# Kernel tuning notes

Hardware: AMD Instinct MI355X
Metric: run time of the kernel (lower is better)

Reference implementation:

```python
import jax, jax.numpy as jnp
import numpy as np

GRID_NUM = 3  # pykan 'grid' (number of intervals)
K = 3         # spline order

def bspline_basis(x, grid, k):
    # Cox-de Boor recursion, matching pykan B_batch with a shared extended grid.
    # x: (N, Din); grid: (G,) extended grid with G = GRID_NUM + 2*k + 1
    x = x[..., None]  # (N, Din, 1)
    B = ((x >= grid[:-1]) & (x < grid[1:])).astype(x.dtype)  # (N, Din, G-1)
    for p in range(1, k + 1):
        left = (x - grid[:-(p + 1)]) / (grid[p:-1] - grid[:-(p + 1)])
        right = (grid[p + 1:] - x) / (grid[p + 1:] - grid[1:-p])
        B = left * B[..., :-1] + right * B[..., 1:]
    return B  # (N, Din, GRID_NUM + k)

def setup_inputs() -> dict:
    key = jax.random.key(0)
    k1, k2, k3 = jax.random.split(key, 3)
    Bsz, S, Din, Dout = 4, 2048, 768, 768
    x = jax.random.normal(k1, (Bsz, S, Din), dtype=jnp.float32)
    # noise-scale-like init for spline coefficients (noise_scale=0.1)
    coef = (0.1 / GRID_NUM) * jax.random.normal(k2, (Dout, Din, GRID_NUM + K), dtype=jnp.float32)
    inv_sqrt_in = np.float32(1.0 / np.sqrt(Din))
    scale_base = inv_sqrt_in + 0.1 * inv_sqrt_in * jax.random.normal(k3, (Dout, Din), dtype=jnp.float32)
    scale_sp = jnp.ones((Dout, Din), dtype=jnp.float32)
    bias = jnp.zeros((Dout,), dtype=jnp.float32)
    return {"x": x, "coef": coef, "scale_base": scale_base, "scale_sp": scale_sp, "bias": bias}

def reference(x, coef, scale_base, scale_sp, bias):
    # x: (B, S, Din) -> flatten tokens as the original module does
    Bsz, S, Din = x.shape
    xf = x.reshape(-1, Din)  # (N, Din)
    # extended grid: linspace(-1,1,GRID_NUM+1) extended by K points each side (h = 2/GRID_NUM)
    h = 2.0 / GRID_NUM
    grid = jnp.arange(-K, GRID_NUM + K + 1, dtype=x.dtype) * h - 1.0  # (GRID_NUM + 2K + 1,)
    basis = bspline_basis(xf, grid, K)  # (N, Din, GRID_NUM+K)
    # per-edge activation: scale_base*silu(x) + scale_sp*spline(x); mask==1; symbolic branch==0
    base = jax.nn.silu(xf) @ scale_base.T  # (N, Dout)
    spline = jnp.einsum('nim,oim->no', basis, scale_sp[:, :, None] * coef)  # (N, Dout)
    out = base + spline + bias  # bias from pykan biases[l].weight
    return out.reshape(Bsz, S, -1)
```

## Files before the change

kernel.cpp:

```cpp
#include <hip/hip_runtime.h>


typedef _Float16 f16;
typedef __attribute__((ext_vector_type(4))) _Float16 f16x4;
typedef __attribute__((ext_vector_type(8))) _Float16 f16x8;
typedef __attribute__((ext_vector_type(4))) float f32x4;

#define NTOK 8192
#define DIN 768
#define DOUT 768
#define KAUG 5376
#define BM 64
#define BN 128
#define BK 32
#define KT (KAUG / BK)
#define NBLK ((NTOK / BM) * (DOUT / BN))

typedef __attribute__((address_space(1))) void gvoid;
typedef __attribute__((address_space(3))) void lvoid;

__device__ __forceinline__ void spline6(float xv, float* __restrict__ B, float& s) {
  s = xv / (1.0f + __expf(-xv));
  const float h = 2.0f / 3.0f;
  float Bb[9];
#pragma unroll
  for (int g = 0; g < 9; ++g) {
    float t0 = (float)(g - 3) * h - 1.0f;
    float t1 = (float)(g - 2) * h - 1.0f;
    Bb[g] = (xv >= t0 && xv < t1) ? 1.0f : 0.0f;
  }
#pragma unroll
  for (int p = 1; p <= 3; ++p) {
    float inv = 1.0f / ((float)p * h);
#pragma unroll
    for (int j = 0; j < 8; ++j) {
      if (j < 9 - p) {
        float tj = (float)(j - 3) * h - 1.0f;
        float tjp1 = (float)(j + p + 1 - 3) * h - 1.0f;
        Bb[j] = (xv - tj) * inv * Bb[j] + (tjp1 - xv) * inv * Bb[j + 1];
      }
    }
  }
#pragma unroll
  for (int m = 0; m < 6; ++m) B[m] = Bb[m];
}

__global__ __launch_bounds__(256) void build_A(const float* __restrict__ x,
                                               f16* __restrict__ Aa) {
  int idx = (blockIdx.x * 256 + threadIdx.x) * 4;
  float4 xv = *(const float4*)(x + idx);
  int n = idx / DIN;
  int i = idx - n * DIN;

  float B0[6], B1[6], B2[6], B3[6];
  float s0, s1, s2, s3;
  spline6(xv.x, B0, s0);
  spline6(xv.y, B1, s1);
  spline6(xv.z, B2, s2);
  spline6(xv.w, B3, s3);

  size_t base = (size_t)n * KAUG + i;
  f16x4 sv = {(f16)s0, (f16)s1, (f16)s2, (f16)s3};
  *(f16x4*)(Aa + base) = sv;
#pragma unroll
  for (int m = 0; m < 6; ++m) {
    f16x4 bv = {(f16)B0[m], (f16)B1[m], (f16)B2[m], (f16)B3[m]};
    *(f16x4*)(Aa + base + (size_t)(m + 1) * DIN) = bv;
  }
}

__global__ __launch_bounds__(256) void build_W(const float* __restrict__ sb,
                                               const float* __restrict__ ssp,
                                               const float* __restrict__ coef,
                                               f16* __restrict__ Wa) {
  int idx = blockIdx.x * 256 + threadIdx.x;
  float b = sb[idx];
  float sp = ssp[idx];
  int o = idx / DIN;
  int i = idx - o * DIN;
  size_t base = (size_t)o * KAUG + i;
  Wa[base] = (f16)b;
#pragma unroll
  for (int m = 0; m < 6; ++m)
    Wa[base + (size_t)(m + 1) * DIN] = (f16)(sp * coef[(size_t)idx * 6 + m]);
}

__global__ __launch_bounds__(256) void kan_gemm(const f16* __restrict__ A,
                                                const f16* __restrict__ W,
                                                const float* __restrict__ bias,
                                                float* __restrict__ out) {
  __shared__ alignas(16) f16 As0[BM * BK];
  __shared__ alignas(16) f16 As1[BM * BK];
  __shared__ alignas(16) f16 Bs0[BN * BK];
  __shared__ alignas(16) f16 Bs1[BN * BK];

  const int tid = threadIdx.x;
  const int wave = tid >> 6;
  const int lane = tid & 63;

  const int bid = blockIdx.x;
  const int wg = (bid & 7) * (NBLK / 8) + (bid >> 3);
  const int col = wg % 6;
  const int panel = wg / 6;
  const int m0 = panel * BM;
  const int n0 = col * BN;

  const int wm = (wave >> 1) * 32;
  const int wn = (wave & 1) * 64;
  const int r = lane & 15;
  const int q = lane >> 4;

  f32x4 acc[2][4] = {};

  const int c0 = wave * 64 + lane;
  const int rowS0 = c0 >> 2, kb0 = c0 & 3;
  const int c1 = c0 + 256;
  const int rowS1 = c1 >> 2, kb1 = c1 & 3;

  const f16* gA0 = A + (size_t)(m0 + rowS0) * KAUG + kb0 * 8;
  const f16* gB0 = W + (size_t)(n0 + rowS0) * KAUG + kb0 * 8;
  const f16* gB1 = W + (size_t)(n0 + rowS1) * KAUG + kb1 * 8;

  const int wo = wave * 512;

#define STAGE(AS, BS, ktile)                                                             \
  do {                                                                                   \
    const int koff = (ktile)*BK;                                                         \
    __builtin_amdgcn_global_load_lds((gvoid*)(gA0 + koff), (lvoid*)(AS + wo), 16, 0, 0); \
    __builtin_amdgcn_global_load_lds((gvoid*)(gB0 + koff), (lvoid*)(BS + wo), 16, 0, 0); \
    __builtin_amdgcn_global_load_lds((gvoid*)(gB1 + koff), (lvoid*)(BS + wo + 2048), 16, \
                                     0, 0);                                              \
  } while (0)

#define COMPUTE(AS, BS)                                                                  \
  do {                                                                                   \
    f16x8 af[2], bf[4];                                                                  \
    _Pragma("unroll") for (int mi = 0; mi < 2; ++mi) af[mi] =                            \
        *(const f16x8*)&AS[(wm + mi * 16 + r) * BK + q * 8];                             \
    _Pragma("unroll") for (int ni = 0; ni < 4; ++ni) bf[ni] =                            \
        *(const f16x8*)&BS[(wn + ni * 16 + r) * BK + q * 8];                             \
    _Pragma("unroll") for (int mi = 0; mi < 2; ++mi) _Pragma("unroll") for (int ni = 0;  \
                                                                            ni < 4;     \
                                                                            ++ni)       \
        acc[mi][ni] =                                                                    \
        __builtin_amdgcn_mfma_f32_16x16x32_f16(af[mi], bf[ni], acc[mi][ni], 0, 0, 0);    \
  } while (0)

  STAGE(As0, Bs0, 0);
  __syncthreads();

  for (int kt = 0; kt < KT; kt += 2) {
    STAGE(As1, Bs1, kt + 1);
    COMPUTE(As0, Bs0);
    __syncthreads();
    if (kt + 2 < KT) STAGE(As0, Bs0, kt + 2);
    COMPUTE(As1, Bs1);
    __syncthreads();
  }

#undef STAGE
#undef COMPUTE

#pragma unroll
  for (int mi = 0; mi < 2; ++mi) {
#pragma unroll
    for (int ni = 0; ni < 4; ++ni) {
      const int gcol = n0 + wn + ni * 16 + r;
      const float bv = bias[gcol];
#pragma unroll
      for (int rg = 0; rg < 4; ++rg) {
        const int grow = m0 + wm + mi * 16 + q * 4 + rg;
        out[(size_t)grow * DOUT + gcol] = acc[mi][ni][rg] + bv;
      }
    }
  }
}

extern "C" void kernel_launch(void* const* d_in, const int* in_sizes, int n_in,
                              void* d_out, int out_size, void* d_ws, size_t ws_size,
                              hipStream_t stream) {
  const float* x = (const float*)d_in[0];
  const float* coef = (const float*)d_in[1];
  const float* scale_base = (const float*)d_in[2];
  const float* scale_sp = (const float*)d_in[3];
  const float* bias = (const float*)d_in[4];
  float* out = (float*)d_out;

  f16* Aa = (f16*)d_ws;
  f16* Wa = (f16*)((char*)d_ws + (size_t)NTOK * KAUG * 2);

  build_A<<<(NTOK * DIN) / (256 * 4), 256, 0, stream>>>(x, Aa);
  build_W<<<(DOUT * DIN) / 256, 256, 0, stream>>>(scale_base, scale_sp, coef, Wa);
  kan_gemm<<<NBLK, 256, 0, stream>>>(Aa, Wa, bias, out);
}
```

Before: 212.1 us.

## Enlarge GEMM tiles, add triple-buffered pipeline with LDS swizzle, merge prep kernels

The GEMM moves to 128x192x64 tiles with 512 threads and a three-stage LDS ring buffer. Global-to-LDS loads are issued two tiles ahead and split across the half-K phases, with XOR-swizzled LDS layout to avoid bank conflicts and setprio around MFMA bursts. The two preprocessing kernels are merged into one launch, and the W build now uses vectorized loads. This aims to raise arithmetic intensity and hide memory latency, at the cost of more LDS and register pressure and fewer blocks (256) on the machine.

```diff
diff --git a/kernel.cpp b/kernel.cpp
--- a/kernel.cpp
+++ b/kernel.cpp
@@ -2,6 +2,7 @@
 
 
 typedef _Float16 f16;
+typedef __attribute__((ext_vector_type(2))) _Float16 f16x2;
 typedef __attribute__((ext_vector_type(4))) _Float16 f16x4;
 typedef __attribute__((ext_vector_type(8))) _Float16 f16x8;
 typedef __attribute__((ext_vector_type(4))) float f32x4;
@@ -10,10 +11,12 @@
 #define DIN 768
 #define DOUT 768
 #define KAUG 5376
-#define BM 64
-#define BN 128
-#define BK 32
-#define KT (KAUG / BK)
+#define BM 128
+#define BN 192
+#define BK 64
+#define NKT (KAUG / BK)
+#define ASZ (BM * BK)
+#define BSZ (BN * BK)
 #define NBLK ((NTOK / BM) * (DOUT / BN))
 
 typedef __attribute__((address_space(1))) void gvoid;
@@ -45,54 +48,65 @@
   for (int m = 0; m < 6; ++m) B[m] = Bb[m];
 }
 
-__global__ __launch_bounds__(256) void build_A(const float* __restrict__ x,
-                                               f16* __restrict__ Aa) {
-  int idx = (blockIdx.x * 256 + threadIdx.x) * 4;
-  float4 xv = *(const float4*)(x + idx);
-  int n = idx / DIN;
-  int i = idx - n * DIN;
-
-  float B0[6], B1[6], B2[6], B3[6];
-  float s0, s1, s2, s3;
-  spline6(xv.x, B0, s0);
-  spline6(xv.y, B1, s1);
-  spline6(xv.z, B2, s2);
-  spline6(xv.w, B3, s3);
-
-  size_t base = (size_t)n * KAUG + i;
-  f16x4 sv = {(f16)s0, (f16)s1, (f16)s2, (f16)s3};
-  *(f16x4*)(Aa + base) = sv;
-#pragma unroll
-  for (int m = 0; m < 6; ++m) {
-    f16x4 bv = {(f16)B0[m], (f16)B1[m], (f16)B2[m], (f16)B3[m]};
-    *(f16x4*)(Aa + base + (size_t)(m + 1) * DIN) = bv;
-  }
-}
-
-__global__ __launch_bounds__(256) void build_W(const float* __restrict__ sb,
-                                               const float* __restrict__ ssp,
-                                               const float* __restrict__ coef,
-                                               f16* __restrict__ Wa) {
-  int idx = blockIdx.x * 256 + threadIdx.x;
-  float b = sb[idx];
-  float sp = ssp[idx];
-  int o = idx / DIN;
-  int i = idx - o * DIN;
-  size_t base = (size_t)o * KAUG + i;
-  Wa[base] = (f16)b;
-#pragma unroll
-  for (int m = 0; m < 6; ++m)
-    Wa[base + (size_t)(m + 1) * DIN] = (f16)(sp * coef[(size_t)idx * 6 + m]);
-}
-
-__global__ __launch_bounds__(256) void kan_gemm(const f16* __restrict__ A,
-                                                const f16* __restrict__ W,
-                                                const float* __restrict__ bias,
-                                                float* __restrict__ out) {
-  __shared__ alignas(16) f16 As0[BM * BK];
-  __shared__ alignas(16) f16 As1[BM * BK];
-  __shared__ alignas(16) f16 Bs0[BN * BK];
-  __shared__ alignas(16) f16 Bs1[BN * BK];
+#define NBLK_A ((NTOK * DIN) / 1024)
+#define NBLK_W ((DOUT * DIN) / 512)
+
+__global__ __launch_bounds__(256) void build_AW(const float* __restrict__ x,
+                                                const float* __restrict__ sb,
+                                                const float* __restrict__ ssp,
+                                                const float* __restrict__ coef,
+                                                f16* __restrict__ Aa,
+                                                f16* __restrict__ Wa) {
+  const int b = blockIdx.x;
+  if (b < NBLK_A) {
+    int idx = (b * 256 + threadIdx.x) * 4;
+    float4 xv = *(const float4*)(x + idx);
+    int n = idx / DIN;
+    int i = idx - n * DIN;
+
+    float B0[6], B1[6], B2[6], B3[6];
+    float s0, s1, s2, s3;
+    spline6(xv.x, B0, s0);
+    spline6(xv.y, B1, s1);
+    spline6(xv.z, B2, s2);
+    spline6(xv.w, B3, s3);
+
+    size_t base = (size_t)n * KAUG + i;
+    f16x4 sv = {(f16)s0, (f16)s1, (f16)s2, (f16)s3};
+    *(f16x4*)(Aa + base) = sv;
+#pragma unroll
+    for (int m = 0; m < 6; ++m) {
+      f16x4 bv = {(f16)B0[m], (f16)B1[m], (f16)B2[m], (f16)B3[m]};
+      *(f16x4*)(Aa + base + (size_t)(m + 1) * DIN) = bv;
+    }
+  } else {
+    int idx2 = ((b - NBLK_A) * 256 + threadIdx.x) * 2;
+    float2 bb = *(const float2*)(sb + idx2);
+    float2 pp = *(const float2*)(ssp + idx2);
+    int o = idx2 / DIN;
+    int i = idx2 - o * DIN;
+    size_t base = (size_t)o * KAUG + i;
+    f16x2 w0 = {(f16)bb.x, (f16)bb.y};
+    *(f16x2*)(Wa + base) = w0;
+    float4 c0 = *(const float4*)(coef + (size_t)idx2 * 6);
+    float4 c1 = *(const float4*)(coef + (size_t)idx2 * 6 + 4);
+    float4 c2 = *(const float4*)(coef + (size_t)idx2 * 6 + 8);
+    float ma[6] = {c0.x, c0.y, c0.z, c0.w, c1.x, c1.y};
+    float mb[6] = {c1.z, c1.w, c2.x, c2.y, c2.z, c2.w};
+#pragma unroll
+    for (int m = 0; m < 6; ++m) {
+      f16x2 wv = {(f16)(pp.x * ma[m]), (f16)(pp.y * mb[m])};
+      *(f16x2*)(Wa + base + (size_t)(m + 1) * DIN) = wv;
+    }
+  }
+}
+
+__global__ __launch_bounds__(512, 2) void kan_gemm(const f16* __restrict__ A,
+                                                   const f16* __restrict__ W,
+                                                   const float* __restrict__ bias,
+                                                   float* __restrict__ out) {
+  __shared__ alignas(16) f16 As[3 * ASZ];
+  __shared__ alignas(16) f16 Bs[3 * BSZ];
 
   const int tid = threadIdx.x;
   const int wave = tid >> 6;
@@ -100,71 +114,113 @@
 
   const int bid = blockIdx.x;
   const int wg = (bid & 7) * (NBLK / 8) + (bid >> 3);
-  const int col = wg % 6;
-  const int panel = wg / 6;
-  const int m0 = panel * BM;
-  const int n0 = col * BN;
-
-  const int wm = (wave >> 1) * 32;
-  const int wn = (wave & 1) * 64;
+  const int m0 = (wg >> 2) * BM;
+  const int n0 = (wg & 3) * BN;
+
+  const int wm = (wave >> 2) * 64;
+  const int wn = (wave & 3) * 48;
   const int r = lane & 15;
   const int q = lane >> 4;
-
-  f32x4 acc[2][4] = {};
-
-  const int c0 = wave * 64 + lane;
-  const int rowS0 = c0 >> 2, kb0 = c0 & 3;
-  const int c1 = c0 + 256;
-  const int rowS1 = c1 >> 2, kb1 = c1 & 3;
-
-  const f16* gA0 = A + (size_t)(m0 + rowS0) * KAUG + kb0 * 8;
-  const f16* gB0 = W + (size_t)(n0 + rowS0) * KAUG + kb0 * 8;
-  const f16* gB1 = W + (size_t)(n0 + rowS1) * KAUG + kb1 * 8;
-
-  const int wo = wave * 512;
-
-#define STAGE(AS, BS, ktile)                                                             \
-  do {                                                                                   \
-    const int koff = (ktile)*BK;                                                         \
-    __builtin_amdgcn_global_load_lds((gvoid*)(gA0 + koff), (lvoid*)(AS + wo), 16, 0, 0); \
-    __builtin_amdgcn_global_load_lds((gvoid*)(gB0 + koff), (lvoid*)(BS + wo), 16, 0, 0); \
-    __builtin_amdgcn_global_load_lds((gvoid*)(gB1 + koff), (lvoid*)(BS + wo + 2048), 16, \
-                                     0, 0);                                              \
-  } while (0)
-
-#define COMPUTE(AS, BS)                                                                  \
-  do {                                                                                   \
-    f16x8 af[2], bf[4];                                                                  \
-    _Pragma("unroll") for (int mi = 0; mi < 2; ++mi) af[mi] =                            \
-        *(const f16x8*)&AS[(wm + mi * 16 + r) * BK + q * 8];                             \
-    _Pragma("unroll") for (int ni = 0; ni < 4; ++ni) bf[ni] =                            \
-        *(const f16x8*)&BS[(wn + ni * 16 + r) * BK + q * 8];                             \
-    _Pragma("unroll") for (int mi = 0; mi < 2; ++mi) _Pragma("unroll") for (int ni = 0;  \
-                                                                            ni < 4;     \
-                                                                            ++ni)       \
-        acc[mi][ni] =                                                                    \
-        __builtin_amdgcn_mfma_f32_16x16x32_f16(af[mi], bf[ni], acc[mi][ni], 0, 0, 0);    \
-  } while (0)
-
-  STAGE(As0, Bs0, 0);
-  __syncthreads();
-
-  for (int kt = 0; kt < KT; kt += 2) {
-    STAGE(As1, Bs1, kt + 1);
-    COMPUTE(As0, Bs0);
-    __syncthreads();
-    if (kt + 2 < KT) STAGE(As0, Bs0, kt + 2);
-    COMPUTE(As1, Bs1);
-    __syncthreads();
-  }
-
-#undef STAGE
-#undef COMPUTE
-
-#pragma unroll
-  for (int mi = 0; mi < 2; ++mi) {
-#pragma unroll
-    for (int ni = 0; ni < 4; ++ni) {
+  const int r7 = r & 7;
+
+  f32x4 acc[4][3] = {};
+
+  const int cA0 = tid, cA1 = tid + 512;
+  const int cB0 = tid, cB1 = tid + 512, cB2 = tid + 1024;
+  const f16* gA0 = A + (size_t)(m0 + (cA0 >> 3)) * KAUG + ((cA0 & 7) ^ ((cA0 >> 3) & 7)) * 8;
+  const f16* gA1 = A + (size_t)(m0 + (cA1 >> 3)) * KAUG + ((cA1 & 7) ^ ((cA1 >> 3) & 7)) * 8;
+  const f16* gB0 = W + (size_t)(n0 + (cB0 >> 3)) * KAUG + ((cB0 & 7) ^ ((cB0 >> 3) & 7)) * 8;
+  const f16* gB1 = W + (size_t)(n0 + (cB1 >> 3)) * KAUG + ((cB1 & 7) ^ ((cB1 >> 3) & 7)) * 8;
+  const f16* gB2 = W + (size_t)(n0 + (cB2 >> 3)) * KAUG + ((cB2 & 7) ^ ((cB2 >> 3) & 7)) * 8;
+  const int dA0 = wave * 512, dA1 = 4096 + wave * 512;
+  const int dB0 = wave * 512, dB1 = 4096 + wave * 512, dB2 = 8192 + wave * 512;
+
+#define STAGE_B(bufi, kt)                                                                  \
+  do {                                                                                     \
+    const int ko = (kt)*BK;                                                                \
+    f16* bb_ = Bs + (bufi)*BSZ;                                                            \
+    __builtin_amdgcn_global_load_lds((gvoid*)(gB0 + ko), (lvoid*)(bb_ + dB0), 16, 0, 0);   \
+    __builtin_amdgcn_global_load_lds((gvoid*)(gB1 + ko), (lvoid*)(bb_ + dB1), 16, 0, 0);   \
+    __builtin_amdgcn_global_load_lds((gvoid*)(gB2 + ko), (lvoid*)(bb_ + dB2), 16, 0, 0);   \
+  } while (0)
+
+#define STAGE_A(bufi, kt)                                                                  \
+  do {                                                                                     \
+    const int ko = (kt)*BK;                                                                \
+    f16* ab_ = As + (bufi)*ASZ;                                                            \
+    __builtin_amdgcn_global_load_lds((gvoid*)(gA0 + ko), (lvoid*)(ab_ + dA0), 16, 0, 0);   \
+    __builtin_amdgcn_global_load_lds((gvoid*)(gA1 + ko), (lvoid*)(ab_ + dA1), 16, 0, 0);   \
+  } while (0)
+
+#define PH(bufi, kh, STAGE_STMT)                                                           \
+  do {                                                                                     \
+    const f16* Ab = As + (bufi)*ASZ;                                                       \
+    const f16* Bb = Bs + (bufi)*BSZ;                                                       \
+    const int sl = (((kh)*4 + q) ^ r7) * 8;                                                \
+    f16x8 af[4], bf[3];                                                                    \
+    _Pragma("unroll") for (int mi = 0; mi < 4; ++mi) af[mi] =                              \
+        *(const f16x8*)&Ab[(wm + mi * 16 + r) * BK + sl];                                  \
+    _Pragma("unroll") for (int ni = 0; ni < 3; ++ni) bf[ni] =                              \
+        *(const f16x8*)&Bb[(wn + ni * 16 + r) * BK + sl];                                  \
+    STAGE_STMT;                                                                            \
+    __builtin_amdgcn_s_setprio(1);                                                         \
+    _Pragma("unroll") for (int mi = 0; mi < 4; ++mi)                                       \
+        _Pragma("unroll") for (int ni = 0; ni < 3; ++ni) acc[mi][ni] =                     \
+        __builtin_amdgcn_mfma_f32_16x16x32_f16(af[mi], bf[ni], acc[mi][ni], 0, 0, 0);      \
+    __builtin_amdgcn_s_setprio(0);                                                         \
+  } while (0)
+
+#define FENCE_BAR(VMC)                                            \
+  do {                                                            \
+    asm volatile("s_waitcnt lgkmcnt(0) vmcnt(" #VMC ")" ::: "memory"); \
+    __builtin_amdgcn_sched_barrier(0);                            \
+    __builtin_amdgcn_s_barrier();                                 \
+  } while (0)
+
+#define MID_BAR()                                                 \
+  do {                                                            \
+    asm volatile("s_waitcnt lgkmcnt(0)" ::: "memory");            \
+    __builtin_amdgcn_sched_barrier(0);                            \
+    __builtin_amdgcn_s_barrier();                                 \
+  } while (0)
+
+  STAGE_B(0, 0);
+  STAGE_A(0, 0);
+  STAGE_B(1, 1);
+  STAGE_A(1, 1);
+  FENCE_BAR(5);
+
+  for (int t = 0; t < NKT - 2; ++t) {
+    const int rb = t % 3;
+    const int pb = (t + 2) % 3;
+    PH(rb, 0, STAGE_B(pb, t + 2));
+    MID_BAR();
+    PH(rb, 1, STAGE_A(pb, t + 2));
+    FENCE_BAR(5);
+  }
+  {
+    const int rb = (NKT - 2) % 3;
+    PH(rb, 0, (void)0);
+    MID_BAR();
+    PH(rb, 1, (void)0);
+    FENCE_BAR(0);
+  }
+  {
+    const int rb = (NKT - 1) % 3;
+    PH(rb, 0, (void)0);
+    PH(rb, 1, (void)0);
+  }
+
+#undef STAGE_A
+#undef STAGE_B
+#undef PH
+#undef FENCE_BAR
+#undef MID_BAR
+
+#pragma unroll
+  for (int mi = 0; mi < 4; ++mi) {
+#pragma unroll
+    for (int ni = 0; ni < 3; ++ni) {
       const int gcol = n0 + wn + ni * 16 + r;
       const float bv = bias[gcol];
 #pragma unroll
@@ -189,7 +245,6 @@
   f16* Aa = (f16*)d_ws;
   f16* Wa = (f16*)((char*)d_ws + (size_t)NTOK * KAUG * 2);
 
-  build_A<<<(NTOK * DIN) / (256 * 4), 256, 0, stream>>>(x, Aa);
-  build_W<<<(DOUT * DIN) / 256, 256, 0, stream>>>(scale_base, scale_sp, coef, Wa);
-  kan_gemm<<<NBLK, 256, 0, stream>>>(Aa, Wa, bias, out);
-}
+  build_AW<<<NBLK_A + NBLK_W, 256, 0, stream>>>(x, scale_base, scale_sp, coef, Aa, Wa);
+  kan_gemm<<<NBLK, 512, 0, stream>>>(Aa, Wa, bias, out);
+}
```

Result: faster. 190.5 us (-10.2%).
